# Kernel tuning notes

Measured on AMD Instinct MI355X. Metric: run time of the kernel, lower is better.

The kernel has to match this reference:

```python
import jax, jax.numpy as jnp
import numpy as np

KERNEL = 3072
STRIDE = 512


def setup_inputs() -> dict:
    key = jax.random.key(0)
    ks = jax.random.split(key, 8)
    B, Cin, L = 8, 4, 524288
    Cout, H = 512, 512
    return {
        "input": jax.random.normal(ks[0], (B, Cin, L), jnp.float32),
        "hidden": jnp.zeros((1, B, H), jnp.float32),
        "conv_w": jax.random.normal(ks[1], (Cout, Cin, KERNEL), jnp.float32) * 0.01,
        "conv_b": jax.random.normal(ks[2], (Cout,), jnp.float32) * 0.01,
        "w_ih": jax.random.normal(ks[3], (3 * H, Cout), jnp.float32) * 0.04,
        "w_hh": jax.random.normal(ks[4], (3 * H, H), jnp.float32) * 0.04,
        "b_ih": jax.random.normal(ks[5], (3 * H,), jnp.float32) * 0.04,
        "b_hh": jax.random.normal(ks[6], (3 * H,), jnp.float32) * 0.04,
    }


def _gru_scan(x_tbc, h0, w_ih, w_hh, b_ih, b_hh):
    # PyTorch GRU cell semantics, batched over B, scanned over T.
    # Precompute input projections for all timesteps: [T, B, 3H]
    gi = jnp.einsum('tbc,gc->tbg', x_tbc, w_ih) + b_ih

    def step(h, gi_t):
        gh = h @ w_hh.T + b_hh  # [B, 3H]
        i_r, i_z, i_n = jnp.split(gi_t, 3, axis=-1)
        h_r, h_z, h_n = jnp.split(gh, 3, axis=-1)
        r = jax.nn.sigmoid(i_r + h_r)
        z = jax.nn.sigmoid(i_z + h_z)
        n = jnp.tanh(i_n + r * h_n)
        h_new = (1.0 - z) * n + z * h
        return h_new, h_new

    hT, ys = jax.lax.scan(step, h0, gi)
    return ys, hT


def reference(input, hidden, conv_w, conv_b, w_ih, w_hh, b_ih, b_hh):
    # Conv1d stem: [B, Cin, L] -> [B, Cout, T]
    out = jax.lax.conv_general_dilated(
        input, conv_w, window_strides=(STRIDE,), padding='VALID',
        dimension_numbers=('NCH', 'OIH', 'NCH'))
    out = out + conv_b[None, :, None]
    # dropout is identity in eval mode
    x = jnp.moveaxis(out, 2, 0)  # [T, B, Cout]
    h0 = hidden[0]  # [B, H]
    ys, hT = _gru_scan(x, h0, w_ih, w_hh, b_ih, b_hh)  # ys: [T, B, H]
    T, B, H = ys.shape
    # torch.cat of T tensors [1, B, H] along dim=1 -> [1, T*B, H]
    return ys.reshape(1, T * B, H), hT[None]
```

## Files before the change

### kernel.cpp

```cpp
#include <hip/hip_runtime.h>
#include <hip/hip_fp16.h>
#include <hip/hip_bf16.h>

#define TSTEPS 1019
#define BATCH 8
#define CIN 4
#define LEN 524288
#define COUT 512
#define HID 512
#define KERN 3072
#define CSTRIDE 512
#define KTOT (CIN * KERN)
#define MROWS (TSTEPS * BATCH)

typedef _Float16 half2_v __attribute__((ext_vector_type(2)));
typedef __attribute__((ext_vector_type(8))) short bf16x8;
typedef __attribute__((ext_vector_type(4))) float f32x4;

#if defined(__has_builtin)
#if __has_builtin(__builtin_amdgcn_fdot2)
#define HAVE_FDOT2 1
#endif
#endif

__device__ __forceinline__ float dot2f(__half2 a, __half2 b, float c) {
#ifdef HAVE_FDOT2
    return __builtin_amdgcn_fdot2(__builtin_bit_cast(half2_v, a),
                                  __builtin_bit_cast(half2_v, b), c, false);
#else
    float2 af = __half22float2(a), bf = __half22float2(b);
    return fmaf(af.y, bf.y, fmaf(af.x, bf.x, c));
#endif
}

struct __align__(16) H2x4 { __half2 x, y, z, w; };

__device__ __forceinline__ short bfc(float x) {
    return (short)__builtin_bit_cast(unsigned short, __float2bfloat16(x));
}

__device__ __forceinline__ void load_lds16(const unsigned short* g, unsigned short* l) {
    __builtin_amdgcn_global_load_lds(
        (const __attribute__((address_space(1))) void*)g,
        (__attribute__((address_space(3))) void*)l, 16, 0, 0);
}

__global__ __launch_bounds__(256) void f2bf_k(
        const float* __restrict__ a, unsigned short* __restrict__ o, int n4) {
    int i = blockIdx.x * blockDim.x + threadIdx.x;
    int stride = gridDim.x * blockDim.x;
    for (; i < n4; i += stride) {
        float4 f = reinterpret_cast<const float4*>(a)[i];
        ushort4 u;
        u.x = (unsigned short)bfc(f.x); u.y = (unsigned short)bfc(f.y);
        u.z = (unsigned short)bfc(f.z); u.w = (unsigned short)bfc(f.w);
        reinterpret_cast<ushort4*>(o)[i] = u;
    }
}

__global__ __launch_bounds__(256, 2) void conv_mfma_k(
        const float* __restrict__ in, const unsigned short* __restrict__ wb,
        const float* __restrict__ bias, unsigned short* __restrict__ out) {
    __shared__ unsigned short At[2][128 * 64];
    __shared__ unsigned short Bt[2][128 * 64];
    const int m0 = blockIdx.y * 128;
    const int n0 = blockIdx.x * 128;
    const int tid = threadIdx.x;
    const int w = tid >> 6, l = tid & 63;
    const int wm = w >> 1, wn = w & 1;
    const int fr = l & 15, fq = l >> 4;

    const int ra = tid >> 1, hh = tid & 1;
    int mA = m0 + ra; if (mA > MROWS - 1) mA = MROWS - 1;
    const int tA = mA >> 3, bA = mA & 7;

    f32x4 acc[4][4] = {};

    const int NT = KTOT / 64;

    {
        const int k0 = 0, ci = 0, kr = 0;
        const float* src = in + (size_t)(bA * CIN + ci) * LEN
                              + (size_t)tA * CSTRIDE + kr + hh * 32;
        #pragma unroll
        for (int cc = 0; cc < 4; ++cc) {
            float4 f0 = reinterpret_cast<const float4*>(src)[cc * 2];
            float4 f1 = reinterpret_cast<const float4*>(src)[cc * 2 + 1];
            bf16x8 v;
            v[0] = bfc(f0.x); v[1] = bfc(f0.y); v[2] = bfc(f0.z); v[3] = bfc(f0.w);
            v[4] = bfc(f1.x); v[5] = bfc(f1.y); v[6] = bfc(f1.z); v[7] = bfc(f1.w);
            const int c = hh * 4 + cc, s = c ^ (ra & 7);
            *reinterpret_cast<bf16x8*>(&At[0][ra * 64 + s * 8]) = v;
        }
        #pragma unroll
        for (int i = 0; i < 4; ++i) {
            const int rb = w * 32 + i * 8 + (l >> 3);
            const int s = l & 7, c = s ^ (rb & 7);
            load_lds16(wb + (size_t)(n0 + rb) * KTOT + k0 + c * 8,
                       &Bt[0][(w * 32 + i * 8) * 64]);
        }
    }
    __syncthreads();

    int cur = 0;
    for (int t = 0; t < NT; ++t) {
        const int nxt = cur ^ 1;
        float4 fA[8];
        const bool more = (t + 1 < NT);
        if (more) {
            const int k0 = (t + 1) * 64;
            const int ci = k0 / KERN, kr = k0 - ci * KERN;
            const float* src = in + (size_t)(bA * CIN + ci) * LEN
                                  + (size_t)tA * CSTRIDE + kr + hh * 32;
            #pragma unroll
            for (int v = 0; v < 8; ++v)
                fA[v] = reinterpret_cast<const float4*>(src)[v];
            #pragma unroll
            for (int i = 0; i < 4; ++i) {
                const int rb = w * 32 + i * 8 + (l >> 3);
                const int s = l & 7, c = s ^ (rb & 7);
                load_lds16(wb + (size_t)(n0 + rb) * KTOT + k0 + c * 8,
                           &Bt[nxt][(w * 32 + i * 8) * 64]);
            }
        }
        #pragma unroll
        for (int ks = 0; ks < 2; ++ks) {
            bf16x8 af[4], bfg[4];
            #pragma unroll
            for (int mf = 0; mf < 4; ++mf) {
                const int rA = wm * 64 + mf * 16 + fr;
                const int cw = ks * 4 + fq, s = cw ^ (rA & 7);
                af[mf] = *reinterpret_cast<const bf16x8*>(&At[cur][rA * 64 + s * 8]);
            }
            #pragma unroll
            for (int nf = 0; nf < 4; ++nf) {
                const int rB = wn * 64 + nf * 16 + fr;
                const int cw = ks * 4 + fq, s = cw ^ (rB & 7);
                bfg[nf] = *reinterpret_cast<const bf16x8*>(&Bt[cur][rB * 64 + s * 8]);
            }
            #pragma unroll
            for (int mf = 0; mf < 4; ++mf)
                #pragma unroll
                for (int nf = 0; nf < 4; ++nf)
                    acc[mf][nf] = __builtin_amdgcn_mfma_f32_16x16x32_bf16(
                        af[mf], bfg[nf], acc[mf][nf], 0, 0, 0);
        }
        if (more) {
            #pragma unroll
            for (int cc = 0; cc < 4; ++cc) {
                float4 f0 = fA[cc * 2], f1 = fA[cc * 2 + 1];
                bf16x8 v;
                v[0] = bfc(f0.x); v[1] = bfc(f0.y); v[2] = bfc(f0.z); v[3] = bfc(f0.w);
                v[4] = bfc(f1.x); v[5] = bfc(f1.y); v[6] = bfc(f1.z); v[7] = bfc(f1.w);
                const int c = hh * 4 + cc, s = c ^ (ra & 7);
                *reinterpret_cast<bf16x8*>(&At[nxt][ra * 64 + s * 8]) = v;
            }
        }
        __syncthreads();
        cur = nxt;
    }

    #pragma unroll
    for (int nf = 0; nf < 4; ++nf) {
        const int n = n0 + wn * 64 + nf * 16 + fr;
        const float bv = bias[n];
        #pragma unroll
        for (int mf = 0; mf < 4; ++mf) {
            #pragma unroll
            for (int i = 0; i < 4; ++i) {
                const int m = m0 + wm * 64 + mf * 16 + fq * 4 + i;
                if (m < MROWS)
                    out[(size_t)m * COUT + n] =
                        (unsigned short)bfc(acc[mf][nf][i] + bv);
            }
        }
    }
}

__global__ __launch_bounds__(256, 2) void proj_mfma_k(
        const unsigned short* __restrict__ A, const unsigned short* __restrict__ wb,
        const float* __restrict__ bias, float* __restrict__ out) {
    __shared__ unsigned short At[2][128 * 64];
    __shared__ unsigned short Bt[2][128 * 64];
    const int m0 = blockIdx.y * 128;
    const int n0 = blockIdx.x * 128;
    const int tid = threadIdx.x;
    const int w = tid >> 6, l = tid & 63;
    const int wm = w >> 1, wn = w & 1;
    const int fr = l & 15, fq = l >> 4;

    f32x4 acc[4][4] = {};
    const int NT = COUT / 64;

    auto stage = [&](int buf, int k0) {
        #pragma unroll
        for (int i = 0; i < 4; ++i) {
            const int r = w * 32 + i * 8 + (l >> 3);
            const int s = l & 7, c = s ^ (r & 7);
            int mA = m0 + r; if (mA > MROWS - 1) mA = MROWS - 1;
            load_lds16(A + (size_t)mA * COUT + k0 + c * 8,
                       &At[buf][(w * 32 + i * 8) * 64]);
            load_lds16(wb + (size_t)(n0 + r) * COUT + k0 + c * 8,
                       &Bt[buf][(w * 32 + i * 8) * 64]);
        }
    };

    stage(0, 0);
    __syncthreads();
    int cur = 0;
    for (int t = 0; t < NT; ++t) {
        const int nxt = cur ^ 1;
        if (t + 1 < NT) stage(nxt, (t + 1) * 64);
        #pragma unroll
        for (int ks = 0; ks < 2; ++ks) {
            bf16x8 af[4], bfg[4];
            #pragma unroll
            for (int mf = 0; mf < 4; ++mf) {
                const int rA = wm * 64 + mf * 16 + fr;
                const int cw = ks * 4 + fq, s = cw ^ (rA & 7);
                af[mf] = *reinterpret_cast<const bf16x8*>(&At[cur][rA * 64 + s * 8]);
            }
            #pragma unroll
            for (int nf = 0; nf < 4; ++nf) {
                const int rB = wn * 64 + nf * 16 + fr;
                const int cw = ks * 4 + fq, s = cw ^ (rB & 7);
                bfg[nf] = *reinterpret_cast<const bf16x8*>(&Bt[cur][rB * 64 + s * 8]);
            }
            #pragma unroll
            for (int mf = 0; mf < 4; ++mf)
                #pragma unroll
                for (int nf = 0; nf < 4; ++nf)
                    acc[mf][nf] = __builtin_amdgcn_mfma_f32_16x16x32_bf16(
                        af[mf], bfg[nf], acc[mf][nf], 0, 0, 0);
        }
        __syncthreads();
        cur = nxt;
    }

    #pragma unroll
    for (int nf = 0; nf < 4; ++nf) {
        const int n = n0 + wn * 64 + nf * 16 + fr;
        const float bv = bias[n];
        #pragma unroll
        for (int mf = 0; mf < 4; ++mf) {
            #pragma unroll
            for (int i = 0; i < 4; ++i) {
                const int m = m0 + wm * 64 + mf * 16 + fq * 4 + i;
                if (m < MROWS)
                    out[(size_t)m * 1536 + n] = acc[mf][nf][i] + bv;
            }
        }
    }
}

__global__ __launch_bounds__(512, 1) void gru_scan_k(
        const float* __restrict__ gi, const float* __restrict__ w_hh,
        const float* __restrict__ b_hh, const float* __restrict__ hidden,
        float* __restrict__ out, unsigned long long* __restrict__ h_ex) {
    const int bid = blockIdx.x;
    const int b   = bid & 7;
    const int isl = bid >> 3;
    const int tid = threadIdx.x;
    const int q   = tid >> 7;
    const int g   = tid & 127;
    const int j   = isl * 128 + g;

    __shared__ __align__(16) __half2 hh2[256];
    __shared__ float p_lds[1920];

    __half2 wreg[3][64];
    #pragma unroll
    for (int m = 0; m < 3; ++m) {
        const float* wp = w_hh + (size_t)(j + m * 512) * HID + q * 128;
        #pragma unroll
        for (int kk = 0; kk < 32; ++kk) {
            float4 v = reinterpret_cast<const float4*>(wp)[kk];
            wreg[m][2 * kk]     = __halves2half2(__float2half_rn(v.x), __float2half_rn(v.y));
            wreg[m][2 * kk + 1] = __halves2half2(__float2half_rn(v.z), __float2half_rn(v.w));
        }
    }

    float bhr = 0.f, bhz = 0.f, bhn = 0.f, hprev = 0.f;
    if (tid < 128) {
        bhr = b_hh[j]; bhz = b_hh[j + 512]; bhn = b_hh[j + 1024];
        hprev = hidden[b * HID + j];
    }
    if (tid < 256) {
        float h0a = hidden[b * HID + 2 * tid];
        float h0b = hidden[b * HID + 2 * tid + 1];
        hh2[tid] = __halves2half2(__float2half(h0a), __float2half(h0b));
    }
    __syncthreads();

    float gir = 0.f, giz = 0.f, gin = 0.f;
    if (tid < 128) {
        const float* gp = gi + (size_t)b * 1536 + j;
        gir = gp[0]; giz = gp[512]; gin = gp[1024];
    }

    for (int t = 0; t < TSTEPS; ++t) {
        const H2x4* hv4 = reinterpret_cast<const H2x4*>(hh2 + q * 64);
        float a0 = 0, a1 = 0, a2 = 0, c0 = 0, c1 = 0, c2 = 0;
        #pragma unroll
        for (int kk = 0; kk < 16; ++kk) {
            H2x4 h4 = hv4[kk];
            a0 = dot2f(wreg[0][4 * kk + 0], h4.x, a0);
            a1 = dot2f(wreg[1][4 * kk + 0], h4.x, a1);
            a2 = dot2f(wreg[2][4 * kk + 0], h4.x, a2);
            c0 = dot2f(wreg[0][4 * kk + 1], h4.y, c0);
            c1 = dot2f(wreg[1][4 * kk + 1], h4.y, c1);
            c2 = dot2f(wreg[2][4 * kk + 1], h4.y, c2);
            a0 = dot2f(wreg[0][4 * kk + 2], h4.z, a0);
            a1 = dot2f(wreg[1][4 * kk + 2], h4.z, a1);
            a2 = dot2f(wreg[2][4 * kk + 2], h4.z, a2);
            c0 = dot2f(wreg[0][4 * kk + 3], h4.w, c0);
            c1 = dot2f(wreg[1][4 * kk + 3], h4.w, c1);
            c2 = dot2f(wreg[2][4 * kk + 3], h4.w, c2);
        }
        p_lds[(0 * 128 + g) * 5 + q] = a0 + c0;
        p_lds[(1 * 128 + g) * 5 + q] = a1 + c1;
        p_lds[(2 * 128 + g) * 5 + q] = a2 + c2;
        __syncthreads();

        float hnew = 0.f;
        if (tid < 128) {
            const float* pr = &p_lds[(0 * 128 + tid) * 5];
            const float* pz = &p_lds[(1 * 128 + tid) * 5];
            const float* pn = &p_lds[(2 * 128 + tid) * 5];
            const float ghr = pr[0] + pr[1] + pr[2] + pr[3] + bhr;
            const float ghz = pz[0] + pz[1] + pz[2] + pz[3] + bhz;
            const float ghn = pn[0] + pn[1] + pn[2] + pn[3] + bhn;
            const float r = 1.f / (1.f + __expf(-(gir + ghr)));
            const float z = 1.f / (1.f + __expf(-(giz + ghz)));
            const float nx = gin + r * ghn;
            const float n = 1.f - 2.f / (__expf(2.f * nx) + 1.f);
            hnew = (1.f - z) * n + z * hprev;
            hprev = hnew;
            out[(size_t)(t * BATCH + b) * HID + j] = hnew;
            float hother = __shfl_xor(hnew, 1);
            if (!(tid & 1) && t < TSTEPS - 1) {
                unsigned long long* pub = h_ex
                    + (size_t)(((t + 1) & 1) * BATCH + b) * 256
                    + isl * 64 + (tid >> 1);
                __half2 h2 = __halves2half2(__float2half(hnew), __float2half(hother));
                unsigned long long v =
                    ((unsigned long long)(unsigned)(t + 1) << 32) |
                    (unsigned long long)__builtin_bit_cast(unsigned, h2);
                __hip_atomic_store(pub, v, __ATOMIC_RELAXED,
                                   __HIP_MEMORY_SCOPE_AGENT);
            }
        }
        if (t == TSTEPS - 1) break;

        if (tid < 128) {
            const float* gp = gi + (size_t)((t + 1) * BATCH + b) * 1536 + j;
            gir = gp[0]; giz = gp[512]; gin = gp[1024];
        }

        if (tid < 256) {
            unsigned long long* src = h_ex
                + (size_t)(((t + 1) & 1) * BATCH + b) * 256 + tid;
            unsigned long long v;
            do {
                v = __hip_atomic_load(src, __ATOMIC_RELAXED,
                                      __HIP_MEMORY_SCOPE_AGENT);
            } while ((unsigned)(v >> 32) != (unsigned)(t + 1));
            hh2[tid] = __builtin_bit_cast(__half2, (unsigned)(v & 0xffffffffu));
        }
        __syncthreads();
    }
    if (tid < 128)
        out[(size_t)TSTEPS * BATCH * HID + b * HID + j] = hprev;
}

extern "C" void kernel_launch(void* const* d_in, const int* in_sizes, int n_in,
                              void* d_out, int out_size, void* d_ws, size_t ws_size,
                              hipStream_t stream) {
    (void)in_sizes; (void)n_in; (void)out_size; (void)ws_size;
    const float* input  = (const float*)d_in[0];
    const float* hidden = (const float*)d_in[1];
    const float* conv_w = (const float*)d_in[2];
    const float* conv_b = (const float*)d_in[3];
    const float* w_ih   = (const float*)d_in[4];
    const float* w_hh   = (const float*)d_in[5];
    const float* b_ih   = (const float*)d_in[6];
    const float* b_hh   = (const float*)d_in[7];
    float* out = (float*)d_out;

    char* ws = (char*)d_ws;
    float*          gi       = (float*)ws;
    unsigned short* conv_out = (unsigned short*)(ws + 50085888);
    unsigned short* w_bf     = (unsigned short*)(ws + 58433536);
    unsigned short* wih_bf   = (unsigned short*)(ws + 71016448);
    unsigned long long* h_ex = (unsigned long long*)(ws + 72589312);

    f2bf_k<<<2048, 256, 0, stream>>>(conv_w, w_bf, KTOT * COUT / 4);
    f2bf_k<<<768, 256, 0, stream>>>(w_ih, wih_bf, 1536 * COUT / 4);

    dim3 cgrid(4, 64);
    conv_mfma_k<<<cgrid, 256, 0, stream>>>(input, w_bf, conv_b, conv_out);

    dim3 pgrid(12, 64);
    proj_mfma_k<<<pgrid, 256, 0, stream>>>(conv_out, wih_bf, b_ih, gi);

    hipMemsetAsync(h_ex, 0, 32768, stream);

    gru_scan_k<<<32, 512, 0, stream>>>(gi, w_hh, b_hh, hidden, out, h_ex);
}
```

Baseline: 2.208 ms.

## Replace second GRU barrier with per-wave polling and local LDS flags

The GRU scan kernel now maps waves so that the waves owning the block's own hidden slice do the gate math and write the new h values straight into the LDS strips. Other waves each poll only their own slice from global memory, and an LDS flag tells the local waves when their slice is ready. This drops the second block-wide barrier and lets waves begin the next matvec as soon as their data arrives, shortening the per-step critical path of the serial scan. It relies on volatile LDS spin-waits and careful ordering between waves, which risks subtle races or deadlock.

```diff
diff --git a/kernel.cpp b/kernel.cpp
--- a/kernel.cpp
+++ b/kernel.cpp
@@ -75,13 +75,11 @@
     const int tA = mA >> 3, bA = mA & 7;
 
     f32x4 acc[4][4] = {};
-
     const int NT = KTOT / 64;
 
     {
-        const int k0 = 0, ci = 0, kr = 0;
-        const float* src = in + (size_t)(bA * CIN + ci) * LEN
-                              + (size_t)tA * CSTRIDE + kr + hh * 32;
+        const float* src = in + (size_t)(bA * CIN + 0) * LEN
+                              + (size_t)tA * CSTRIDE + 0 + hh * 32;
         #pragma unroll
         for (int cc = 0; cc < 4; ++cc) {
             float4 f0 = reinterpret_cast<const float4*>(src)[cc * 2];
@@ -96,7 +94,7 @@
         for (int i = 0; i < 4; ++i) {
             const int rb = w * 32 + i * 8 + (l >> 3);
             const int s = l & 7, c = s ^ (rb & 7);
-            load_lds16(wb + (size_t)(n0 + rb) * KTOT + k0 + c * 8,
+            load_lds16(wb + (size_t)(n0 + rb) * KTOT + 0 + c * 8,
                        &Bt[0][(w * 32 + i * 8) * 64]);
         }
     }
@@ -261,12 +259,16 @@
     const int b   = bid & 7;
     const int isl = bid >> 3;
     const int tid = threadIdx.x;
-    const int q   = tid >> 7;
-    const int g   = tid & 127;
+    const int wv  = tid >> 6;
+    const int l   = tid & 63;
+    const int q   = wv >> 1;
+    const int g   = (wv & 1) * 64 + l;
     const int j   = isl * 128 + g;
-
-    __shared__ __align__(16) __half2 hh2[256];
-    __shared__ float p_lds[1920];
+    const bool is_gate = (q == isl);
+
+    __shared__ __align__(16) __half2 strip[8][64];
+    __shared__ float p_lds[3 * 128 * 5];
+    __shared__ int lflag[2];
 
     __half2 wreg[3][64];
     #pragma unroll
@@ -281,25 +283,40 @@
     }
 
     float bhr = 0.f, bhz = 0.f, bhn = 0.f, hprev = 0.f;
-    if (tid < 128) {
+    float gir = 0.f, giz = 0.f, gin = 0.f;
+    if (is_gate) {
         bhr = b_hh[j]; bhz = b_hh[j + 512]; bhn = b_hh[j + 1024];
         hprev = hidden[b * HID + j];
-    }
-    if (tid < 256) {
-        float h0a = hidden[b * HID + 2 * tid];
-        float h0b = hidden[b * HID + 2 * tid + 1];
-        hh2[tid] = __halves2half2(__float2half(h0a), __float2half(h0b));
-    }
+        gir = gi[(size_t)b * 1536 + j];
+        giz = gi[(size_t)b * 1536 + j + 512];
+        gin = gi[(size_t)b * 1536 + j + 1024];
+    }
+    if (tid < 2) lflag[tid] = 0;
+    strip[wv][l] = __halves2half2(__float2half(hidden[b * HID + q * 128 + 2 * l]),
+                                  __float2half(hidden[b * HID + q * 128 + 2 * l + 1]));
     __syncthreads();
 
-    float gir = 0.f, giz = 0.f, gin = 0.f;
-    if (tid < 128) {
-        const float* gp = gi + (size_t)b * 1536 + j;
-        gir = gp[0]; giz = gp[512]; gin = gp[1024];
-    }
-
     for (int t = 0; t < TSTEPS; ++t) {
-        const H2x4* hv4 = reinterpret_cast<const H2x4*>(hh2 + q * 64);
+        if (t > 0) {
+            if (!is_gate) {
+                const unsigned long long* src =
+                    h_ex + (size_t)((t & 1) * BATCH + b) * 256 + q * 64 + l;
+                unsigned long long v;
+                do {
+                    v = __hip_atomic_load(src, __ATOMIC_RELAXED,
+                                          __HIP_MEMORY_SCOPE_AGENT);
+                } while ((unsigned)(v >> 32) != (unsigned)t);
+                strip[wv][l] =
+                    __builtin_bit_cast(__half2, (unsigned)(v & 0xffffffffu));
+                asm volatile("s_waitcnt lgkmcnt(0)" ::: "memory");
+            } else {
+                volatile int* f0 = &lflag[0];
+                volatile int* f1 = &lflag[1];
+                while (*f0 < t || *f1 < t) {}
+                asm volatile("" ::: "memory");
+            }
+        }
+        const H2x4* hv4 = reinterpret_cast<const H2x4*>(&strip[wv][0]);
         float a0 = 0, a1 = 0, a2 = 0, c0 = 0, c1 = 0, c2 = 0;
         #pragma unroll
         for (int kk = 0; kk < 16; ++kk) {
@@ -322,54 +339,45 @@
         p_lds[(2 * 128 + g) * 5 + q] = a2 + c2;
         __syncthreads();
 
-        float hnew = 0.f;
-        if (tid < 128) {
-            const float* pr = &p_lds[(0 * 128 + tid) * 5];
-            const float* pz = &p_lds[(1 * 128 + tid) * 5];
-            const float* pn = &p_lds[(2 * 128 + tid) * 5];
-            const float ghr = pr[0] + pr[1] + pr[2] + pr[3] + bhr;
-            const float ghz = pz[0] + pz[1] + pz[2] + pz[3] + bhz;
-            const float ghn = pn[0] + pn[1] + pn[2] + pn[3] + bhn;
-            const float r = 1.f / (1.f + __expf(-(gir + ghr)));
-            const float z = 1.f / (1.f + __expf(-(giz + ghz)));
-            const float nx = gin + r * ghn;
-            const float n = 1.f - 2.f / (__expf(2.f * nx) + 1.f);
-            hnew = (1.f - z) * n + z * hprev;
+        if (is_gate) {
+            const float* pr = &p_lds[(0 * 128 + g) * 5];
+            const float* pz = &p_lds[(1 * 128 + g) * 5];
+            const float* pn = &p_lds[(2 * 128 + g) * 5];
+            const float ghr = (pr[0] + pr[1]) + (pr[2] + pr[3]) + bhr;
+            const float ghz = (pz[0] + pz[1]) + (pz[2] + pz[3]) + bhz;
+            const float ghn = (pn[0] + pn[1]) + (pn[2] + pn[3]) + bhn;
+            const float rr = 1.f / (1.f + __expf(-(gir + ghr)));
+            const float zz = 1.f / (1.f + __expf(-(giz + ghz)));
+            const float nx = gin + rr * ghn;
+            const float nn = 1.f - 2.f / (__expf(2.f * nx) + 1.f);
+            const float hnew = (1.f - zz) * nn + zz * hprev;
             hprev = hnew;
-            out[(size_t)(t * BATCH + b) * HID + j] = hnew;
-            float hother = __shfl_xor(hnew, 1);
-            if (!(tid & 1) && t < TSTEPS - 1) {
-                unsigned long long* pub = h_ex
-                    + (size_t)(((t + 1) & 1) * BATCH + b) * 256
-                    + isl * 64 + (tid >> 1);
-                __half2 h2 = __halves2half2(__float2half(hnew), __float2half(hother));
-                unsigned long long v =
-                    ((unsigned long long)(unsigned)(t + 1) << 32) |
-                    (unsigned long long)__builtin_bit_cast(unsigned, h2);
-                __hip_atomic_store(pub, v, __ATOMIC_RELAXED,
-                                   __HIP_MEMORY_SCOPE_AGENT);
-            }
-        }
-        if (t == TSTEPS - 1) break;
-
-        if (tid < 128) {
-            const float* gp = gi + (size_t)((t + 1) * BATCH + b) * 1536 + j;
-            gir = gp[0]; giz = gp[512]; gin = gp[1024];
-        }
-
-        if (tid < 256) {
-            unsigned long long* src = h_ex
-                + (size_t)(((t + 1) & 1) * BATCH + b) * 256 + tid;
-            unsigned long long v;
-            do {
-                v = __hip_atomic_load(src, __ATOMIC_RELAXED,
-                                      __HIP_MEMORY_SCOPE_AGENT);
-            } while ((unsigned)(v >> 32) != (unsigned)(t + 1));
-            hh2[tid] = __builtin_bit_cast(__half2, (unsigned)(v & 0xffffffffu));
-        }
-        __syncthreads();
-    }
-    if (tid < 128)
+            const float hother = __shfl_xor(hnew, 1);
+            if (t + 1 < TSTEPS) {
+                if (!(g & 1)) {
+                    const __half2 h2 = __halves2half2(__float2half(hnew),
+                                                      __float2half(hother));
+                    const unsigned long long v =
+                        ((unsigned long long)(unsigned)(t + 1) << 32) |
+                        (unsigned long long)__builtin_bit_cast(unsigned, h2);
+                    __hip_atomic_store(
+                        h_ex + (size_t)(((t + 1) & 1) * BATCH + b) * 256
+                             + isl * 64 + (g >> 1),
+                        v, __ATOMIC_RELAXED, __HIP_MEMORY_SCOPE_AGENT);
+                    strip[2 * isl][g >> 1] = h2;
+                    strip[2 * isl + 1][g >> 1] = h2;
+                }
+                asm volatile("s_waitcnt lgkmcnt(0)" ::: "memory");
+                if (l == 0) lflag[wv & 1] = t + 1;
+                out[(size_t)(t * BATCH + b) * HID + j] = hnew;
+                const float* gp = gi + (size_t)((t + 1) * BATCH + b) * 1536 + j;
+                gir = gp[0]; giz = gp[512]; gin = gp[1024];
+            } else {
+                out[(size_t)(t * BATCH + b) * HID + j] = hnew;
+            }
+        }
+    }
+    if (is_gate)
         out[(size_t)TSTEPS * BATCH * HID + b * HID + j] = hprev;
 }
 
```

New measurement: 2.129 ms. -3.6%, faster.
